# Kernel tuning notes

Measured on AMD Instinct MI355X. Metric: run time of the kernel, lower is better.

The kernel has to match this reference:

```python
import jax, jax.numpy as jnp
import numpy as np
import math

LAMBDA_ATTRACT = 2.5
REPEL_STRENGTH = 0.15
EPSILON = 0.1  # repulsion distance offset
NORM_EPS = 1e-8
TAU_WEIGHT = 0.3
N = 8192


def _pairwise_angular(theta):
    # angular_distance(theta_i, theta_j) = min(|a-b|, 2*pi - |a-b|), shape [n, n]
    diff = jnp.abs(theta[:, None] - theta[None, :])
    return jnp.minimum(diff, 2.0 * math.pi - diff)


def setup_inputs() -> dict:
    key = jax.random.key(0)
    k1, k2 = jax.random.split(key)
    theta = jax.random.uniform(k1, (N,), dtype=jnp.float32, minval=-math.pi, maxval=math.pi)
    tau = jax.random.normal(k2, (N,), dtype=jnp.float32)
    return {"theta": theta, "tau": tau}


def reference(theta, tau):
    n = theta.shape[0]
    eye = jnp.eye(n, dtype=bool)

    d_theta = _pairwise_angular(theta)                      # [n, n]
    d_tau = jnp.abs(tau[:, None] - tau[None, :])            # [n, n]
    dist = d_theta + TAU_WEIGHT * d_tau

    # attention: exp(-lambda * dist), diagonal excluded, row-normalized
    dist_no_self = jnp.where(eye, jnp.inf, dist)
    scores = jnp.exp(-LAMBDA_ATTRACT * dist_no_self)
    attn = scores / jnp.sum(scores, axis=1, keepdims=True)

    cos_part = jnp.cos(theta)
    sin_part = jnp.sin(theta)
    R_x = attn @ cos_part
    R_y = attn @ sin_part

    # vectorized O(n^2) repulsion (replaces the python double loop)
    d = d_theta + EPSILON
    strength = REPEL_STRENGTH / (d * d)                     # [n, n]
    dx = cos_part[:, None] - cos_part[None, :]
    dy = sin_part[:, None] - sin_part[None, :]
    norm = jnp.sqrt(dx * dx + dy * dy) + NORM_EPS
    inv = jnp.where(eye, 0.0, strength / norm)              # mask i == j
    repel_force_x = jnp.sum(inv * dx, axis=1)
    repel_force_y = jnp.sum(inv * dy, axis=1)

    force_x = R_x + repel_force_x
    force_y = R_y + repel_force_y
    theta_out = jnp.arctan2(force_y, force_x)
    tau_out = attn @ tau
    return (theta_out, tau_out, attn)
```

## Files before the change

### kernel.cpp

```cpp
#include <hip/hip_runtime.h>
#include <math.h>

#define N_PTS 8192
#define TPB 256
#define RPB 4

#define C_LAMBDA   2.5f
#define C_REPEL    0.15f
#define C_EPS      0.1f
#define C_NORM_EPS 1e-8f
#define C_TAUW     0.3f
#define C_TWO_PI   6.28318530717958647692f
#define C_NEG_L_LOG2E (-3.60673760222240625f)
#define C_Q_DELTA  1e-16f

typedef float vf4 __attribute__((ext_vector_type(4)));

__device__ __forceinline__ float fast_exp2(float x) {
#if __has_builtin(__builtin_amdgcn_exp2f)
    return __builtin_amdgcn_exp2f(x);
#else
    return exp2f(x);
#endif
}
__device__ __forceinline__ float fast_rsqrt(float x) {
#if __has_builtin(__builtin_amdgcn_rsqf)
    return __builtin_amdgcn_rsqf(x);
#else
    return rsqrtf(x);
#endif
}
__device__ __forceinline__ float fast_log2(float x) {
#if __has_builtin(__builtin_amdgcn_logf)
    return __builtin_amdgcn_logf(x);
#else
    return log2f(x);
#endif
}

__device__ __forceinline__ float wave_reduce_sum(float v) {
    #pragma unroll
    for (int off = 32; off > 0; off >>= 1)
        v += __shfl_down(v, off, 64);
    return v;
}

__global__ void pack_kernel(const float* __restrict__ theta,
                            const float* __restrict__ tau,
                            float4* __restrict__ pk,
                            float2* __restrict__ pk2) {
    int i = blockIdx.x * blockDim.x + threadIdx.x;
    float t = theta[i];
    float u = tau[i];
    pk[i]  = make_float4(t, u, cosf(t), sinf(t));
    pk2[i] = make_float2(t, u);
}

__global__ __launch_bounds__(TPB) void fused_kernel(
    const float4* __restrict__ pk,
    const float4* __restrict__ pq,
    float* __restrict__ out)
{
    const int tid  = threadIdx.x;
    const int row0 = blockIdx.x * RPB;

    float th_i[RPB], ta_i[RPB], c_i[RPB], s_i[RPB];
    #pragma unroll
    for (int r = 0; r < RPB; ++r) {
        float4 p = pk[row0 + r];
        th_i[r] = p.x; ta_i[r] = p.y; c_i[r] = p.z; s_i[r] = p.w;
    }

    float a_sum[RPB], a_x[RPB], a_y[RPB], a_t[RPB], rp_x[RPB], rp_y[RPB];
    #pragma unroll
    for (int r = 0; r < RPB; ++r) {
        a_sum[r] = 0.f; a_x[r] = 0.f; a_y[r] = 0.f;
        a_t[r] = 0.f; rp_x[r] = 0.f; rp_y[r] = 0.f;
    }

    #pragma unroll 4
    for (int k = 0; k < N_PTS / TPB; ++k) {
        float4 cur = pk[tid + k * TPB];
        #pragma unroll
        for (int r = 0; r < RPB; ++r) {
            float ad    = fabsf(th_i[r] - cur.x);
            float dth   = fminf(ad, C_TWO_PI - ad);
            float t     = fmaf(fabsf(ta_i[r] - cur.y), C_TAUW, dth);
            float score = fast_exp2(t * C_NEG_L_LOG2E);
            a_sum[r] += score;
            a_x[r]   = fmaf(score, cur.z, a_x[r]);
            a_y[r]   = fmaf(score, cur.w, a_y[r]);
            a_t[r]   = fmaf(score, cur.y, a_t[r]);

            float d   = dth + C_EPS;
            float dx  = c_i[r] - cur.z;
            float dy  = s_i[r] - cur.w;
            float q   = fmaf(dx, dx, dy * dy);
            float d2  = d * d;
            float inv = fast_rsqrt((q + C_Q_DELTA) * (d2 * d2));
            rp_x[r] = fmaf(inv, dx, rp_x[r]);
            rp_y[r] = fmaf(inv, dy, rp_y[r]);
        }
    }

    __shared__ float red[RPB][6][TPB / 64];
    __shared__ float l2s[RPB];
    const int wave = tid >> 6;
    const int lane = tid & 63;
    #pragma unroll
    for (int r = 0; r < RPB; ++r) {
        float v0 = wave_reduce_sum(a_sum[r]);
        float v1 = wave_reduce_sum(a_x[r]);
        float v2 = wave_reduce_sum(a_y[r]);
        float v3 = wave_reduce_sum(a_t[r]);
        float v4 = wave_reduce_sum(rp_x[r]);
        float v5 = wave_reduce_sum(rp_y[r]);
        if (lane == 0) {
            red[r][0][wave] = v0; red[r][1][wave] = v1; red[r][2][wave] = v2;
            red[r][3][wave] = v3; red[r][4][wave] = v4; red[r][5][wave] = v5;
        }
    }
    __syncthreads();

    if (tid < RPB) {
        const int r = tid;
        float s = 0.f, x = 0.f, y = 0.f, t = 0.f, rx = 0.f, ry = 0.f;
        #pragma unroll
        for (int w = 0; w < TPB / 64; ++w) {
            s  += red[r][0][w]; x  += red[r][1][w]; y  += red[r][2][w];
            t  += red[r][3][w]; rx += red[r][4][w]; ry += red[r][5][w];
        }
        float4 p = pk[row0 + r];
        s -= 1.0f;
        x -= p.z;
        y -= p.w;
        t -= p.y;
        float invr = 1.0f / s;
        float fx = fmaf(x, invr, C_REPEL * rx);
        float fy = fmaf(y, invr, C_REPEL * ry);
        out[row0 + r]         = atan2f(fy, fx);
        out[N_PTS + row0 + r] = t * invr;
        l2s[r] = fast_log2(invr);
    }
    __syncthreads();

    float l2r[RPB];
    #pragma unroll
    for (int r = 0; r < RPB; ++r) l2r[r] = l2s[r];

    float* __restrict__ attn = out + 2 * N_PTS;

    #pragma unroll 2
    for (int k = 0; k < N_PTS / (TPB * 4); ++k) {
        const int base = tid + k * TPB;
        float4 f1 = pq[2 * base];
        float4 f2 = pq[2 * base + 1];
        const int j0 = 4 * base;
        #pragma unroll
        for (int r = 0; r < RPB; ++r) {
            float ad0  = fabsf(th_i[r] - f1.x);
            float dth0 = fminf(ad0, C_TWO_PI - ad0);
            float t0   = fmaf(fabsf(ta_i[r] - f1.y), C_TAUW, dth0);
            float v0   = fast_exp2(fmaf(t0, C_NEG_L_LOG2E, l2r[r]));

            float ad1  = fabsf(th_i[r] - f1.z);
            float dth1 = fminf(ad1, C_TWO_PI - ad1);
            float t1   = fmaf(fabsf(ta_i[r] - f1.w), C_TAUW, dth1);
            float v1   = fast_exp2(fmaf(t1, C_NEG_L_LOG2E, l2r[r]));

            float ad2  = fabsf(th_i[r] - f2.x);
            float dth2 = fminf(ad2, C_TWO_PI - ad2);
            float t2   = fmaf(fabsf(ta_i[r] - f2.y), C_TAUW, dth2);
            float v2   = fast_exp2(fmaf(t2, C_NEG_L_LOG2E, l2r[r]));

            float ad3  = fabsf(th_i[r] - f2.z);
            float dth3 = fminf(ad3, C_TWO_PI - ad3);
            float t3   = fmaf(fabsf(ta_i[r] - f2.w), C_TAUW, dth3);
            float v3   = fast_exp2(fmaf(t3, C_NEG_L_LOG2E, l2r[r]));

            vf4 o = {v0, v1, v2, v3};
            __builtin_nontemporal_store(o, (vf4*)(attn + (size_t)(row0 + r) * N_PTS + j0));
        }
    }

    __syncthreads();
    if (tid < RPB) {
        const int i = row0 + tid;
        attn[(size_t)i * N_PTS + i] = 0.0f;
    }
}

extern "C" void kernel_launch(void* const* d_in, const int* in_sizes, int n_in,
                              void* d_out, int out_size, void* d_ws, size_t ws_size,
                              hipStream_t stream) {
    const float* theta = (const float*)d_in[0];
    const float* tau   = (const float*)d_in[1];

    float4* pk  = (float4*)d_ws;
    float2* pk2 = (float2*)((char*)d_ws + 128 * 1024);
    float*  out = (float*)d_out;

    pack_kernel<<<N_PTS / 256, 256, 0, stream>>>(theta, tau, pk, pk2);
    fused_kernel<<<N_PTS / RPB, TPB, 0, stream>>>(pk, (const float4*)pk2, out);
}
```

Measured before the change: 285.8 us.

## Interleave attention-row stores with next group's reduction pass in software pipeline

Each block now handles two groups of four rows. The compute-heavy reduction pass for the second group runs in the same loop as the bandwidth-heavy attention writes for the first group, so ALU work and memory stores overlap inside one wave. The second group's rows are then written out alone. Nontemporal stores are replaced with ordinary stores, and the block count is halved, which lowers parallelism and may raise register pressure.

```diff
diff --git a/kernel.cpp b/kernel.cpp
--- a/kernel.cpp
+++ b/kernel.cpp
@@ -3,7 +3,8 @@
 
 #define N_PTS 8192
 #define TPB 256
-#define RPB 4
+#define GRP 4
+#define RPB (2 * GRP)
 
 #define C_LAMBDA   2.5f
 #define C_REPEL    0.15f
@@ -44,6 +45,32 @@
         v += __shfl_down(v, off, 64);
     return v;
 }
+
+#define A_BODY(cur, TH, TA, CC, SS, AS, AX, AY, AT, RX, RY) do {           \
+    float ad    = fabsf((TH) - (cur).x);                                   \
+    float dth   = fminf(ad, C_TWO_PI - ad);                                \
+    float t     = fmaf(fabsf((TA) - (cur).y), C_TAUW, dth);                \
+    float score = fast_exp2(t * C_NEG_L_LOG2E);                            \
+    (AS) += score;                                                         \
+    (AX)  = fmaf(score, (cur).z, (AX));                                    \
+    (AY)  = fmaf(score, (cur).w, (AY));                                    \
+    (AT)  = fmaf(score, (cur).y, (AT));                                    \
+    float d   = dth + C_EPS;                                               \
+    float dx  = (CC) - (cur).z;                                            \
+    float dy  = (SS) - (cur).w;                                            \
+    float q   = fmaf(dx, dx, dy * dy);                                     \
+    float d2  = d * d;                                                     \
+    float inv = fast_rsqrt((q + C_Q_DELTA) * (d2 * d2));                   \
+    (RX) = fmaf(inv, dx, (RX));                                            \
+    (RY) = fmaf(inv, dy, (RY));                                            \
+} while (0)
+
+#define B_VAL(THJ, TAJ, THB, TAB, L2B, V) do {                             \
+    float ad  = fabsf((THB) - (THJ));                                      \
+    float dth = fminf(ad, C_TWO_PI - ad);                                  \
+    float t   = fmaf(fabsf((TAB) - (TAJ)), C_TAUW, dth);                   \
+    (V) = fast_exp2(fmaf(t, C_NEG_L_LOG2E, (L2B)));                        \
+} while (0)
 
 __global__ void pack_kernel(const float* __restrict__ theta,
                             const float* __restrict__ tau,
@@ -63,58 +90,42 @@
 {
     const int tid  = threadIdx.x;
     const int row0 = blockIdx.x * RPB;
-
-    float th_i[RPB], ta_i[RPB], c_i[RPB], s_i[RPB];
-    #pragma unroll
-    for (int r = 0; r < RPB; ++r) {
+    const int wave = tid >> 6;
+    const int lane = tid & 63;
+
+    __shared__ float red[GRP][6][TPB / 64];
+    __shared__ float l2sA[GRP];
+    __shared__ float l2sB[GRP];
+
+    float* __restrict__ attn = out + 2 * N_PTS;
+
+    float th[GRP], ta[GRP], cc[GRP], ss[GRP];
+    float aS[GRP], aX[GRP], aY[GRP], aT[GRP], rX[GRP], rY[GRP];
+    #pragma unroll
+    for (int r = 0; r < GRP; ++r) {
         float4 p = pk[row0 + r];
-        th_i[r] = p.x; ta_i[r] = p.y; c_i[r] = p.z; s_i[r] = p.w;
-    }
-
-    float a_sum[RPB], a_x[RPB], a_y[RPB], a_t[RPB], rp_x[RPB], rp_y[RPB];
-    #pragma unroll
-    for (int r = 0; r < RPB; ++r) {
-        a_sum[r] = 0.f; a_x[r] = 0.f; a_y[r] = 0.f;
-        a_t[r] = 0.f; rp_x[r] = 0.f; rp_y[r] = 0.f;
+        th[r] = p.x; ta[r] = p.y; cc[r] = p.z; ss[r] = p.w;
+        aS[r] = 0.f; aX[r] = 0.f; aY[r] = 0.f;
+        aT[r] = 0.f; rX[r] = 0.f; rY[r] = 0.f;
     }
 
     #pragma unroll 4
     for (int k = 0; k < N_PTS / TPB; ++k) {
         float4 cur = pk[tid + k * TPB];
         #pragma unroll
-        for (int r = 0; r < RPB; ++r) {
-            float ad    = fabsf(th_i[r] - cur.x);
-            float dth   = fminf(ad, C_TWO_PI - ad);
-            float t     = fmaf(fabsf(ta_i[r] - cur.y), C_TAUW, dth);
-            float score = fast_exp2(t * C_NEG_L_LOG2E);
-            a_sum[r] += score;
-            a_x[r]   = fmaf(score, cur.z, a_x[r]);
-            a_y[r]   = fmaf(score, cur.w, a_y[r]);
-            a_t[r]   = fmaf(score, cur.y, a_t[r]);
-
-            float d   = dth + C_EPS;
-            float dx  = c_i[r] - cur.z;
-            float dy  = s_i[r] - cur.w;
-            float q   = fmaf(dx, dx, dy * dy);
-            float d2  = d * d;
-            float inv = fast_rsqrt((q + C_Q_DELTA) * (d2 * d2));
-            rp_x[r] = fmaf(inv, dx, rp_x[r]);
-            rp_y[r] = fmaf(inv, dy, rp_y[r]);
-        }
-    }
-
-    __shared__ float red[RPB][6][TPB / 64];
-    __shared__ float l2s[RPB];
-    const int wave = tid >> 6;
-    const int lane = tid & 63;
-    #pragma unroll
-    for (int r = 0; r < RPB; ++r) {
-        float v0 = wave_reduce_sum(a_sum[r]);
-        float v1 = wave_reduce_sum(a_x[r]);
-        float v2 = wave_reduce_sum(a_y[r]);
-        float v3 = wave_reduce_sum(a_t[r]);
-        float v4 = wave_reduce_sum(rp_x[r]);
-        float v5 = wave_reduce_sum(rp_y[r]);
+        for (int r = 0; r < GRP; ++r)
+            A_BODY(cur, th[r], ta[r], cc[r], ss[r],
+                   aS[r], aX[r], aY[r], aT[r], rX[r], rY[r]);
+    }
+
+    #pragma unroll
+    for (int r = 0; r < GRP; ++r) {
+        float v0 = wave_reduce_sum(aS[r]);
+        float v1 = wave_reduce_sum(aX[r]);
+        float v2 = wave_reduce_sum(aY[r]);
+        float v3 = wave_reduce_sum(aT[r]);
+        float v4 = wave_reduce_sum(rX[r]);
+        float v5 = wave_reduce_sum(rY[r]);
         if (lane == 0) {
             red[r][0][wave] = v0; red[r][1][wave] = v1; red[r][2][wave] = v2;
             red[r][3][wave] = v3; red[r][4][wave] = v4; red[r][5][wave] = v5;
@@ -122,7 +133,7 @@
     }
     __syncthreads();
 
-    if (tid < RPB) {
+    if (tid < GRP) {
         const int r = tid;
         float s = 0.f, x = 0.f, y = 0.f, t = 0.f, rx = 0.f, ry = 0.f;
         #pragma unroll
@@ -132,54 +143,103 @@
         }
         float4 p = pk[row0 + r];
         s -= 1.0f;
-        x -= p.z;
-        y -= p.w;
-        t -= p.y;
+        x -= p.z;  y -= p.w;  t -= p.y;
         float invr = 1.0f / s;
         float fx = fmaf(x, invr, C_REPEL * rx);
         float fy = fmaf(y, invr, C_REPEL * ry);
         out[row0 + r]         = atan2f(fy, fx);
         out[N_PTS + row0 + r] = t * invr;
-        l2s[r] = fast_log2(invr);
-    }
-    __syncthreads();
-
-    float l2r[RPB];
-    #pragma unroll
-    for (int r = 0; r < RPB; ++r) l2r[r] = l2s[r];
-
-    float* __restrict__ attn = out + 2 * N_PTS;
-
-    #pragma unroll 2
-    for (int k = 0; k < N_PTS / (TPB * 4); ++k) {
-        const int base = tid + k * TPB;
-        float4 f1 = pq[2 * base];
-        float4 f2 = pq[2 * base + 1];
-        const int j0 = 4 * base;
+        l2sA[r] = fast_log2(invr);
+    }
+    __syncthreads();
+
+    #pragma unroll
+    for (int r = 0; r < GRP; ++r) {
+        float4 p = pk[row0 + GRP + r];
+        th[r] = p.x; ta[r] = p.y; cc[r] = p.z; ss[r] = p.w;
+        aS[r] = 0.f; aX[r] = 0.f; aY[r] = 0.f;
+        aT[r] = 0.f; rX[r] = 0.f; rY[r] = 0.f;
+    }
+
+    #pragma unroll 1
+    for (int rb = 0; rb < GRP; ++rb) {
+        float4 pr  = pk[row0 + rb];
+        float  thb = pr.x, tab = pr.y;
+        float  l2b = l2sA[rb];
+        float* __restrict__ rowp = attn + (size_t)(row0 + rb) * N_PTS;
+        #pragma unroll 1
+        for (int kk = 0; kk < N_PTS / (TPB * 4); ++kk) {
+            float4 cur = pk[tid + (rb * (N_PTS / (TPB * 4)) + kk) * TPB];
+            #pragma unroll
+            for (int r = 0; r < GRP; ++r)
+                A_BODY(cur, th[r], ta[r], cc[r], ss[r],
+                       aS[r], aX[r], aY[r], aT[r], rX[r], rY[r]);
+            const int base = tid + kk * TPB;
+            float4 f1 = pq[2 * base];
+            float4 f2 = pq[2 * base + 1];
+            float v0, v1, v2, v3;
+            B_VAL(f1.x, f1.y, thb, tab, l2b, v0);
+            B_VAL(f1.z, f1.w, thb, tab, l2b, v1);
+            B_VAL(f2.x, f2.y, thb, tab, l2b, v2);
+            B_VAL(f2.z, f2.w, thb, tab, l2b, v3);
+            vf4 o = {v0, v1, v2, v3};
+            *(vf4*)(rowp + 4 * base) = o;
+        }
+    }
+
+    #pragma unroll
+    for (int r = 0; r < GRP; ++r) {
+        float v0 = wave_reduce_sum(aS[r]);
+        float v1 = wave_reduce_sum(aX[r]);
+        float v2 = wave_reduce_sum(aY[r]);
+        float v3 = wave_reduce_sum(aT[r]);
+        float v4 = wave_reduce_sum(rX[r]);
+        float v5 = wave_reduce_sum(rY[r]);
+        if (lane == 0) {
+            red[r][0][wave] = v0; red[r][1][wave] = v1; red[r][2][wave] = v2;
+            red[r][3][wave] = v3; red[r][4][wave] = v4; red[r][5][wave] = v5;
+        }
+    }
+    __syncthreads();
+
+    if (tid < GRP) {
+        const int r = tid;
+        float s = 0.f, x = 0.f, y = 0.f, t = 0.f, rx = 0.f, ry = 0.f;
         #pragma unroll
-        for (int r = 0; r < RPB; ++r) {
-            float ad0  = fabsf(th_i[r] - f1.x);
-            float dth0 = fminf(ad0, C_TWO_PI - ad0);
-            float t0   = fmaf(fabsf(ta_i[r] - f1.y), C_TAUW, dth0);
-            float v0   = fast_exp2(fmaf(t0, C_NEG_L_LOG2E, l2r[r]));
-
-            float ad1  = fabsf(th_i[r] - f1.z);
-            float dth1 = fminf(ad1, C_TWO_PI - ad1);
-            float t1   = fmaf(fabsf(ta_i[r] - f1.w), C_TAUW, dth1);
-            float v1   = fast_exp2(fmaf(t1, C_NEG_L_LOG2E, l2r[r]));
-
-            float ad2  = fabsf(th_i[r] - f2.x);
-            float dth2 = fminf(ad2, C_TWO_PI - ad2);
-            float t2   = fmaf(fabsf(ta_i[r] - f2.y), C_TAUW, dth2);
-            float v2   = fast_exp2(fmaf(t2, C_NEG_L_LOG2E, l2r[r]));
-
-            float ad3  = fabsf(th_i[r] - f2.z);
-            float dth3 = fminf(ad3, C_TWO_PI - ad3);
-            float t3   = fmaf(fabsf(ta_i[r] - f2.w), C_TAUW, dth3);
-            float v3   = fast_exp2(fmaf(t3, C_NEG_L_LOG2E, l2r[r]));
-
+        for (int w = 0; w < TPB / 64; ++w) {
+            s  += red[r][0][w]; x  += red[r][1][w]; y  += red[r][2][w];
+            t  += red[r][3][w]; rx += red[r][4][w]; ry += red[r][5][w];
+        }
+        float4 p = pk[row0 + GRP + r];
+        s -= 1.0f;
+        x -= p.z;  y -= p.w;  t -= p.y;
+        float invr = 1.0f / s;
+        float fx = fmaf(x, invr, C_REPEL * rx);
+        float fy = fmaf(y, invr, C_REPEL * ry);
+        out[row0 + GRP + r]         = atan2f(fy, fx);
+        out[N_PTS + row0 + GRP + r] = t * invr;
+        l2sB[r] = fast_log2(invr);
+    }
+    __syncthreads();
+
+    #pragma unroll 1
+    for (int rb = 0; rb < GRP; ++rb) {
+        float4 pr  = pk[row0 + GRP + rb];
+        float  thb = pr.x, tab = pr.y;
+        float  l2b = l2sB[rb];
+        float* __restrict__ rowp = attn + (size_t)(row0 + GRP + rb) * N_PTS;
+        #pragma unroll 2
+        for (int kk = 0; kk < N_PTS / (TPB * 4); ++kk) {
+            const int base = tid + kk * TPB;
+            float4 f1 = pq[2 * base];
+            float4 f2 = pq[2 * base + 1];
+            float v0, v1, v2, v3;
+            B_VAL(f1.x, f1.y, thb, tab, l2b, v0);
+            B_VAL(f1.z, f1.w, thb, tab, l2b, v1);
+            B_VAL(f2.x, f2.y, thb, tab, l2b, v2);
+            B_VAL(f2.z, f2.w, thb, tab, l2b, v3);
             vf4 o = {v0, v1, v2, v3};
-            __builtin_nontemporal_store(o, (vf4*)(attn + (size_t)(row0 + r) * N_PTS + j0));
+            *(vf4*)(rowp + 4 * base) = o;
         }
     }
 
```

After: 285.9 us. About the same (+0.0%).
